# Optimization experiments

Measured on AMD Instinct MI355X. Metric: run time of the kernel, lower is better.

The kernel has to match this reference:

```python
import jax, jax.numpy as jnp
from jax import lax
import numpy as np

B, N, C, NPOINT, K = 8, 4096, 64, 1024, 32
EPS = 1e-5
SLOPE = 0.1  # leakyrelu negative_slope


def setup_inputs() -> dict:
    key = jax.random.key(0)
    ks = jax.random.split(key, 8)
    d = {
        "xyz": jax.random.normal(ks[0], (B, N, 3), jnp.float32),
        "features": jax.random.normal(ks[1], (B, N, C), jnp.float32),
    }
    for i, n in enumerate(["w_t", "w1_0", "w2_0", "w1_1", "w2_1"]):
        d[n] = jax.random.normal(ks[2 + i], (C, C), jnp.float32) * 0.05
    for n in ["b_t", "b1_0", "b2_0", "b1_1", "b2_1"]:
        d[n] = jnp.zeros((C,), jnp.float32)
    for n in ["g_t", "g1_0", "g2_0", "g1_1", "g2_1"]:
        d[n] = jnp.ones((C,), jnp.float32)
    for n in ["beta_t", "beta1_0", "beta2_0", "beta1_1", "beta2_1"]:
        d[n] = jnp.zeros((C,), jnp.float32)
    return d


def leaky(x):
    return jnp.where(x >= 0, x, SLOPE * x)


def conv1(x, w, b):  # x: [M, Cin, K], w: [Cout, Cin] (1x1 conv)
    return jnp.einsum('mck,oc->mok', x, w) + b[None, :, None]


def bn(x, g, be):  # training-mode BatchNorm1d over (batch, spatial)
    mean = x.mean(axis=(0, 2), keepdims=True)
    var = x.var(axis=(0, 2), keepdims=True)
    return g[None, :, None] * (x - mean) / jnp.sqrt(var + EPS) + be[None, :, None]


def fps(xyz, npoint):
    """Farthest point sampling, deterministic start at index 0. -> [B, npoint] int32"""
    b, n, _ = xyz.shape
    def step(carry, _):
        dist, far = carry
        centroid = jnp.take_along_axis(xyz, far[:, None, None], axis=1)  # [B,1,3]
        d = jnp.sum((xyz - centroid) ** 2, -1)  # [B,N]
        dist = jnp.minimum(dist, d)
        return (dist, jnp.argmax(dist, -1)), far
    init = (jnp.full((b, n), 1e10, xyz.dtype), jnp.zeros((b,), jnp.int32))
    _, idxs = lax.scan(step, init, None, length=npoint)  # [npoint, B]
    return idxs.T


def sqdist(src, dst):  # [B,S,3],[B,N,3] -> [B,S,N]
    d = -2.0 * jnp.einsum('bsc,bnc->bsn', src, dst)
    d += jnp.sum(src ** 2, -1)[:, :, None]
    d += jnp.sum(dst ** 2, -1)[:, None, :]
    return d


def resblock(x, w1, b1, g1, be1, w2, b2, g2, be2):
    h = leaky(bn(conv1(x, w1, b1), g1, be1))
    h = bn(conv1(h, w2, b2), g2, be2)
    return leaky(h + x)


def reference(xyz, features, w_t, b_t, g_t, beta_t,
              w1_0, b1_0, g1_0, beta1_0, w2_0, b2_0, g2_0, beta2_0,
              w1_1, b1_1, g1_1, beta1_1, w2_1, b2_1, g2_1, beta2_1):
    fps_idx = fps(xyz, NPOINT)                                   # [B,S]
    new_xyz = jnp.take_along_axis(xyz, fps_idx[:, :, None], axis=1)  # [B,S,3]
    d = sqdist(new_xyz, xyz)                                     # [B,S,N]
    _, idx = lax.top_k(-d, K)                                    # k smallest -> [B,S,K]
    grouped = jax.vmap(lambda f, i: f[i])(features, idx)         # [B,S,K,C]
    x = grouped.transpose(0, 1, 3, 2).reshape(B * NPOINT, C, K)  # [B*S, C, K]
    x = leaky(bn(conv1(x, w_t, b_t), g_t, beta_t))
    x = resblock(x, w1_0, b1_0, g1_0, beta1_0, w2_0, b2_0, g2_0, beta2_0)
    x = resblock(x, w1_1, b1_1, g1_1, beta1_1, w2_1, b2_1, g2_1, beta2_1)
    nf = x.reshape(B, NPOINT, C, K).transpose(0, 2, 1, 3)        # [B,C,S,K]
    sub_features = nf.max(axis=-1)                               # [B,C,S]
    return (new_xyz.transpose(0, 2, 1), sub_features)
```

## Files before the change

### kernel.cpp

```cpp
#include <hip/hip_runtime.h>
#include <stdint.h>

#define NB 8
#define NN 4096
#define NC 64
#define NS 1024
#define NK 32
#define NQ (NB*NS)
#define NP (NQ*NK)
#define EPSBN 1e-5f

typedef unsigned long long u64;
typedef unsigned short u16;
typedef float v2f __attribute__((ext_vector_type(2)));
typedef short bf8_t __attribute__((ext_vector_type(8)));
typedef float f4_t __attribute__((ext_vector_type(4)));

__device__ __forceinline__ float lrelu(float x){ return x >= 0.0f ? x : 0.1f*x; }

__device__ __forceinline__ unsigned int fkey(float d){
    unsigned int fb = __float_as_uint(d);
    return (fb & 0x80000000u) ? ~fb : (fb | 0x80000000u);
}
__device__ __forceinline__ unsigned f2bf(float f){
    unsigned u = __float_as_uint(f);
    return (u + 0x7fffu + ((u >> 16) & 1u)) >> 16;
}
__device__ __forceinline__ float bflo(unsigned u){ return __uint_as_float(u << 16); }
__device__ __forceinline__ float bfhi(unsigned u){ return __uint_as_float(u & 0xffff0000u); }

__device__ __forceinline__ int wave_incl_add(int x){
    int v = x;
    {int o=__builtin_amdgcn_update_dpp(0,v,0x111,0xf,0xf,true); v+=o;}
    {int o=__builtin_amdgcn_update_dpp(0,v,0x112,0xf,0xf,true); v+=o;}
    {int o=__builtin_amdgcn_update_dpp(0,v,0x114,0xf,0xf,true); v+=o;}
    {int o=__builtin_amdgcn_update_dpp(0,v,0x118,0xf,0xf,true); v+=o;}
    {int o=__builtin_amdgcn_update_dpp(0,v,0x142,0xa,0xf,true); v+=o;}
    {int o=__builtin_amdgcn_update_dpp(0,v,0x143,0xc,0xf,true); v+=o;}
    return v;
}
__device__ __forceinline__ float row_sum16(float x){
    int v = __float_as_int(x);
    {int o=__builtin_amdgcn_update_dpp(0,v,0x111,0xf,0xf,true); v=__float_as_int(__int_as_float(v)+__int_as_float(o));}
    {int o=__builtin_amdgcn_update_dpp(0,v,0x112,0xf,0xf,true); v=__float_as_int(__int_as_float(v)+__int_as_float(o));}
    {int o=__builtin_amdgcn_update_dpp(0,v,0x114,0xf,0xf,true); v=__float_as_int(__int_as_float(v)+__int_as_float(o));}
    {int o=__builtin_amdgcn_update_dpp(0,v,0x118,0xf,0xf,true); v=__float_as_int(__int_as_float(v)+__int_as_float(o));}
    return __int_as_float(v);
}
__device__ __forceinline__ double wave_max_d(double x){
    int lo = __double2loint(x), hi = __double2hiint(x);
    #define FPS_STG(ctl) { \
        int nl=__builtin_amdgcn_update_dpp(lo,lo,ctl,0xf,0xf,false); \
        int nh=__builtin_amdgcn_update_dpp(hi,hi,ctl,0xf,0xf,false); \
        double mx=fmax(__hiloint2double(hi,lo), __hiloint2double(nh,nl)); \
        lo=__double2loint(mx); hi=__double2hiint(mx); }
    FPS_STG(0x111) FPS_STG(0x112) FPS_STG(0x114) FPS_STG(0x118) FPS_STG(0x142) FPS_STG(0x143)
    #undef FPS_STG
    int flo = __builtin_amdgcn_readlane(lo, 63);
    int fhi = __builtin_amdgcn_readlane(hi, 63);
    return __hiloint2double(fhi, flo);
}

__global__ __launch_bounds__(256,1) void fps_kernel(const float* __restrict__ xyz,
                                                    float* __restrict__ out0,
                                                    float* __restrict__ nxyz)
{
    __shared__ float sX[NN], sY[NN], sZ[NN];
    __shared__ double slots[2][4];
    __shared__ int sFar[NS];
    const int b = blockIdx.x, t = threadIdx.x;
    const int lane = t & 63, wv = t >> 6;
    const float* base = xyz + (size_t)b*NN*3;
    for (int i = t; i < NN; i += 256){
        const float* pp = base + 3*i;
        sX[i] = pp[0]; sY[i] = pp[1]; sZ[i] = pp[2];
    }
    __syncthreads();
    v2f PX[8], PY[8], PZ[8], D[8];
    int LO[16];
    const int pb = t*16;
    #pragma unroll
    for (int j = 0; j < 8; ++j){
        PX[j] = (v2f){ sX[pb+2*j], sX[pb+2*j+1] };
        PY[j] = (v2f){ sY[pb+2*j], sY[pb+2*j+1] };
        PZ[j] = (v2f){ sZ[pb+2*j], sZ[pb+2*j+1] };
        D[j]  = (v2f){ 1e10f, 1e10f };
    }
    #pragma unroll
    for (int j = 0; j < 16; ++j) LO[j] = (int)(~(unsigned)(pb + j));
    int far = 0;
    float cx = sX[0], cy = sY[0], cz = sZ[0];
    for (int s = 0; s < NS; ++s){
        if (t == 255) sFar[s] = far;
        double best;
        {
            #pragma clang fp contract(off)
            v2f cx2 = (v2f){cx, cx}, cy2 = (v2f){cy, cy}, cz2 = (v2f){cz, cz};
            best = -1.0;
            #pragma unroll
            for (int j = 0; j < 8; ++j){
                v2f dx = PX[j] - cx2;
                v2f dy = PY[j] - cy2;
                v2f dz = PZ[j] - cz2;
                v2f dd = (dx*dx + dy*dy) + dz*dz;
                v2f nd = __builtin_elementwise_min(D[j], dd);
                D[j] = nd;
                best = fmax(best, __hiloint2double(__float_as_int(nd.x), LO[2*j]));
                best = fmax(best, __hiloint2double(__float_as_int(nd.y), LO[2*j+1]));
            }
        }
        double wb = wave_max_d(best);
        const int par = s & 1;
        if (lane == 0) slots[par][wv] = wb;
        __syncthreads();
        double s0 = slots[par][0], s1 = slots[par][1];
        double s2 = slots[par][2], s3 = slots[par][3];
        double mm = fmax(fmax(s0, s1), fmax(s2, s3));
        far = (int)(~(unsigned)__double2loint(mm));
        cx = sX[far]; cy = sY[far]; cz = sZ[far];
    }
    __syncthreads();
    for (int s = t; s < NS; s += 256){
        const int f = sFar[s];
        const float x = sX[f], y = sY[f], z = sZ[f];
        float* npq = nxyz + ((size_t)b*NS + s)*3;
        npq[0]=x; npq[1]=y; npq[2]=z;
        out0[(b*3+0)*NS+s]=x; out0[(b*3+1)*NS+s]=y; out0[(b*3+2)*NS+s]=z;
    }
}

__global__ __launch_bounds__(256,2) void knn_kernel(const float* __restrict__ xyz,
                                                    const float* __restrict__ nxyz,
                                                    int* __restrict__ kidx)
{
    const int t = threadIdx.x, lane = t & 63, w = t >> 6;
    const int q = blockIdx.x*4 + w;
    const int b = q >> 10;
    const float* base = xyz + (size_t)b*NN*3;
    const float* qp = nxyz + (size_t)q*3;
    const float qx = qp[0], qy = qp[1], qz = qp[2];
    const float qsq = __fadd_rn(__fadd_rn(__fmul_rn(qx,qx),__fmul_rn(qy,qy)),__fmul_rn(qz,qz));

    unsigned int key[64];
    #pragma unroll
    for (int i = 0; i < 64; ++i){
        const int idx = (i<<6) + lane;
        const float* pp = base + 3*idx;
        float x = pp[0], y = pp[1], z = pp[2];
        float dot = __fadd_rn(__fadd_rn(__fmul_rn(qx,x),__fmul_rn(qy,y)),__fmul_rn(qz,z));
        float psq = __fadd_rn(__fadd_rn(__fmul_rn(x,x),__fmul_rn(y,y)),__fmul_rn(z,z));
        float d = __fadd_rn(__fadd_rn(__fmul_rn(-2.0f,dot),qsq),psq);
        key[i] = fkey(d);
    }
    unsigned int pref = 0; int need = 32;
    for (int bit = 31; bit >= 0; --bit){
        const unsigned int bound = 1u << bit;
        int c = 0;
        #pragma unroll
        for (int i = 0; i < 64; ++i) c += ((key[i] ^ pref) < bound) ? 1 : 0;
        int tot = __builtin_amdgcn_readlane(wave_incl_add(c), 63);
        if (tot < need){ need -= tot; pref |= bound; }
    }
    const unsigned int T = pref;
    int cl = 0;
    #pragma unroll
    for (int i = 0; i < 64; ++i) cl += (key[i] < T) ? 1 : 0;
    int incl_cl = wave_incl_add(cl);
    int clx = incl_cl - cl;
    int tiebase = __builtin_amdgcn_readlane(incl_cl, 63);
    int* oq = kidx + (size_t)q*NK;
    int pos = clx;
    #pragma unroll
    for (int i = 0; i < 64; ++i){
        if (key[i] < T){ oq[pos] = (i<<6) + lane; ++pos; }
    }
    int tcount = 0;
    for (int i = 0; i < 64 && tcount < need; ++i){
        u64 m = __ballot(key[i] == T);
        int myrank = (int)__popcll(m & ((1ull << lane) - 1ull));
        if ((key[i] == T) && (tcount + myrank < need))
            oq[tiebase + tcount + myrank] = (i<<6) + lane;
        tcount += (int)__popcll(m);
    }
}

__global__ __launch_bounds__(256) void wtrans_kernel(const float* __restrict__ w0,
    const float* __restrict__ w1, const float* __restrict__ w2,
    const float* __restrict__ w3, const float* __restrict__ w4,
    u16* __restrict__ dst)
{
    const float* s;
    switch (blockIdx.x){
        case 0: s = w0; break; case 1: s = w1; break; case 2: s = w2; break;
        case 3: s = w3; break; default: s = w4; break;
    }
    u16* d = dst + (size_t)blockIdx.x*4096;
    for (int i = threadIdx.x; i < 4096; i += 256){
        const int f = i >> 9, lane = (i >> 3) & 63, j = i & 7;
        const int mt = f >> 1, h = f & 1;
        const int o = mt*16 + (lane & 15);
        const int c = h*32 + (lane >> 4)*8 + j;
        d[i] = (u16)f2bf(s[o*64 + c]);
    }
}

__global__ __launch_bounds__(1024) void finalize_kernel(const float* __restrict__ pin,
    const float* __restrict__ g, const float* __restrict__ beta, float* __restrict__ aff)
{
    __shared__ float l1[1024];
    const int t = threadIdx.x;
    const int stat = t & 127, seg = t >> 7;
    float S = 0.0f;
    #pragma unroll 8
    for (int r = seg*128; r < seg*128 + 128; ++r) S += pin[r*128 + stat];
    l1[t] = S;
    __syncthreads();
    if (t < 128){
        float s = l1[t] + l1[128+t] + l1[256+t] + l1[384+t]
                + l1[512+t] + l1[640+t] + l1[768+t] + l1[896+t];
        l1[t] = s;
    }
    __syncthreads();
    if (t < 64){
        float mean = l1[t] * (1.0f/(float)NP);
        float var  = fmaxf(l1[64+t] * (1.0f/(float)NP) - mean*mean, 0.0f);
        float sc = g[t] * rsqrtf(var + EPSBN);
        aff[t]    = sc;
        aff[64+t] = beta[t] - mean*sc;
    }
}

template<int ACT>
__global__ __launch_bounds__(256,3) void conv_mfma_kernel(const u16* __restrict__ in,
    u16* __restrict__ out, const u16* __restrict__ wfrag, const float* __restrict__ bias,
    const float* __restrict__ aff, float* __restrict__ pout)
{
    __shared__ float sStat[4*128];
    const int t = threadIdx.x, lane = t & 63, wv = t >> 6;
    const int n = lane & 15, q = lane >> 4;
    const int bb = blockIdx.x;

    float scr[16], shr[16];
    if (ACT){
        #pragma unroll
        for (int h = 0; h < 2; ++h){
            float4 a0 = *(const float4*)(aff + h*32 + q*8);
            float4 a1 = *(const float4*)(aff + h*32 + q*8 + 4);
            float4 b0 = *(const float4*)(aff + 64 + h*32 + q*8);
            float4 b1 = *(const float4*)(aff + 64 + h*32 + q*8 + 4);
            scr[h*8+0]=a0.x; scr[h*8+1]=a0.y; scr[h*8+2]=a0.z; scr[h*8+3]=a0.w;
            scr[h*8+4]=a1.x; scr[h*8+5]=a1.y; scr[h*8+6]=a1.z; scr[h*8+7]=a1.w;
            shr[h*8+0]=b0.x; shr[h*8+1]=b0.y; shr[h*8+2]=b0.z; shr[h*8+3]=b0.w;
            shr[h*8+4]=b1.x; shr[h*8+5]=b1.y; shr[h*8+6]=b1.z; shr[h*8+7]=b1.w;
        }
    }
    bf8_t wf[8];
    #pragma unroll
    for (int f = 0; f < 8; ++f)
        wf[f] = *(const bf8_t*)(wfrag + (f*64 + lane)*8);
    f4_t bv[4];
    #pragma unroll
    for (int mt = 0; mt < 4; ++mt)
        bv[mt] = *(const f4_t*)(bias + mt*16 + q*4);

    float st1[16], st2[16];
    #pragma unroll
    for (int e = 0; e < 16; ++e){ st1[e] = 0.0f; st2[e] = 0.0f; }

    #pragma unroll
    for (int i = 0; i < 4; ++i){
        const int p0 = bb*256 + wv*64 + i*16;
        const u16* row = in + (size_t)(p0 + n)*64;
        bf8_t bf0, bf1;
        if (ACT){
            union { unsigned u[4]; bf8_t v; } B0, B1;
            uint4 r0 = *(const uint4*)(row + q*8);
            uint4 r1 = *(const uint4*)(row + 32 + q*8);
            const unsigned ra[4] = {r0.x, r0.y, r0.z, r0.w};
            const unsigned rb[4] = {r1.x, r1.y, r1.z, r1.w};
            #pragma unroll
            for (int d = 0; d < 4; ++d){
                float x0 = bflo(ra[d]), x1 = bfhi(ra[d]);
                float y0 = fmaf(scr[2*d],   x0, shr[2*d]);   y0 = lrelu(y0);
                float y1 = fmaf(scr[2*d+1], x1, shr[2*d+1]); y1 = lrelu(y1);
                B0.u[d] = f2bf(y0) | (f2bf(y1) << 16);
                float z0 = bflo(rb[d]), z1 = bfhi(rb[d]);
                float w0 = fmaf(scr[8+2*d],   z0, shr[8+2*d]);   w0 = lrelu(w0);
                float w1 = fmaf(scr[8+2*d+1], z1, shr[8+2*d+1]); w1 = lrelu(w1);
                B1.u[d] = f2bf(w0) | (f2bf(w1) << 16);
            }
            bf0 = B0.v; bf1 = B1.v;
        } else {
            bf0 = *(const bf8_t*)(row + q*8);
            bf1 = *(const bf8_t*)(row + 32 + q*8);
        }
        f4_t acc[4];
        #pragma unroll
        for (int mt = 0; mt < 4; ++mt){
            acc[mt] = (f4_t){0.f,0.f,0.f,0.f};
            acc[mt] = __builtin_amdgcn_mfma_f32_16x16x32_bf16(wf[mt*2+0], bf0, acc[mt], 0,0,0);
            acc[mt] = __builtin_amdgcn_mfma_f32_16x16x32_bf16(wf[mt*2+1], bf1, acc[mt], 0,0,0);
        }
        u16* orow = out + (size_t)(p0 + n)*64;
        #pragma unroll
        for (int mt = 0; mt < 4; ++mt){
            float v0 = acc[mt].x + bv[mt].x;
            float v1 = acc[mt].y + bv[mt].y;
            float v2 = acc[mt].z + bv[mt].z;
            float v3 = acc[mt].w + bv[mt].w;
            st1[mt*4+0] += v0; st2[mt*4+0] += v0*v0;
            st1[mt*4+1] += v1; st2[mt*4+1] += v1*v1;
            st1[mt*4+2] += v2; st2[mt*4+2] += v2*v2;
            st1[mt*4+3] += v3; st2[mt*4+3] += v3*v3;
            uint2 pk;
            pk.x = f2bf(v0) | (f2bf(v1) << 16);
            pk.y = f2bf(v2) | (f2bf(v3) << 16);
            *(uint2*)(orow + mt*16 + q*4) = pk;
        }
    }
    #pragma unroll
    for (int e = 0; e < 16; ++e){
        float r1 = row_sum16(st1[e]);
        float r2 = row_sum16(st2[e]);
        if (n == 15){
            const int ch = (e >> 2)*16 + q*4 + (e & 3);
            sStat[wv*128 + ch]      = r1;
            sStat[wv*128 + 64 + ch] = r2;
        }
    }
    __syncthreads();
    if (t < 128){
        float s = sStat[t] + sStat[128+t] + sStat[256+t] + sStat[384+t];
        pout[(size_t)bb*128 + t] = s;
    }
}

__global__ __launch_bounds__(256,3) void gconv_mfma_kernel(const float* __restrict__ features,
    const int* __restrict__ kidx, u16* __restrict__ out,
    const u16* __restrict__ wfrag, const float* __restrict__ bias,
    float* __restrict__ pout)
{
    __shared__ float sStat[4*128];
    const int t = threadIdx.x, lane = t & 63, wv = t >> 6;
    const int n = lane & 15, q = lane >> 4;
    const int bb = blockIdx.x;

    bf8_t wf[8];
    #pragma unroll
    for (int f = 0; f < 8; ++f)
        wf[f] = *(const bf8_t*)(wfrag + (f*64 + lane)*8);
    f4_t bv[4];
    #pragma unroll
    for (int mt = 0; mt < 4; ++mt)
        bv[mt] = *(const f4_t*)(bias + mt*16 + q*4);

    float st1[16], st2[16];
    #pragma unroll
    for (int e = 0; e < 16; ++e){ st1[e] = 0.0f; st2[e] = 0.0f; }

    #pragma unroll
    for (int i = 0; i < 4; ++i){
        const int p0 = bb*256 + wv*64 + i*16;
        const int p = p0 + n;
        const int b = p >> 15;
        const int idx = kidx[p];
        const float* frow = features + ((size_t)b*NN + idx)*NC;
        union { unsigned u[4]; bf8_t v; } B0, B1;
        {
            float4 a0 = *(const float4*)(frow + q*8);
            float4 a1 = *(const float4*)(frow + q*8 + 4);
            B0.u[0] = f2bf(a0.x) | (f2bf(a0.y) << 16);
            B0.u[1] = f2bf(a0.z) | (f2bf(a0.w) << 16);
            B0.u[2] = f2bf(a1.x) | (f2bf(a1.y) << 16);
            B0.u[3] = f2bf(a1.z) | (f2bf(a1.w) << 16);
            float4 c0 = *(const float4*)(frow + 32 + q*8);
            float4 c1 = *(const float4*)(frow + 32 + q*8 + 4);
            B1.u[0] = f2bf(c0.x) | (f2bf(c0.y) << 16);
            B1.u[1] = f2bf(c0.z) | (f2bf(c0.w) << 16);
            B1.u[2] = f2bf(c1.x) | (f2bf(c1.y) << 16);
            B1.u[3] = f2bf(c1.z) | (f2bf(c1.w) << 16);
        }
        f4_t acc[4];
        #pragma unroll
        for (int mt = 0; mt < 4; ++mt){
            acc[mt] = (f4_t){0.f,0.f,0.f,0.f};
            acc[mt] = __builtin_amdgcn_mfma_f32_16x16x32_bf16(wf[mt*2+0], B0.v, acc[mt], 0,0,0);
            acc[mt] = __builtin_amdgcn_mfma_f32_16x16x32_bf16(wf[mt*2+1], B1.v, acc[mt], 0,0,0);
        }
        u16* orow = out + (size_t)p*64;
        #pragma unroll
        for (int mt = 0; mt < 4; ++mt){
            float v0 = acc[mt].x + bv[mt].x;
            float v1 = acc[mt].y + bv[mt].y;
            float v2 = acc[mt].z + bv[mt].z;
            float v3 = acc[mt].w + bv[mt].w;
            st1[mt*4+0] += v0; st2[mt*4+0] += v0*v0;
            st1[mt*4+1] += v1; st2[mt*4+1] += v1*v1;
            st1[mt*4+2] += v2; st2[mt*4+2] += v2*v2;
            st1[mt*4+3] += v3; st2[mt*4+3] += v3*v3;
            uint2 pk;
            pk.x = f2bf(v0) | (f2bf(v1) << 16);
            pk.y = f2bf(v2) | (f2bf(v3) << 16);
            *(uint2*)(orow + mt*16 + q*4) = pk;
        }
    }
    #pragma unroll
    for (int e = 0; e < 16; ++e){
        float r1 = row_sum16(st1[e]);
        float r2 = row_sum16(st2[e]);
        if (n == 15){
            const int ch = (e >> 2)*16 + q*4 + (e & 3);
            sStat[wv*128 + ch]      = r1;
            sStat[wv*128 + 64 + ch] = r2;
        }
    }
    __syncthreads();
    if (t < 128){
        float s = sStat[t] + sStat[128+t] + sStat[256+t] + sStat[384+t];
        pout[(size_t)bb*128 + t] = s;
    }
}

__global__ __launch_bounds__(256,2) void resid_kernel(const u16* __restrict__ v,
    const u16* __restrict__ yt, u16* __restrict__ x2,
    const float* __restrict__ affV, const float* __restrict__ affY)
{
    const int t = threadIdx.x;
    const int dc = t & 31, rg = t >> 5;
    const int c0 = dc*2, c1 = c0 + 1;
    const float va0 = affV[c0], vb0 = affV[64+c0];
    const float va1 = affV[c1], vb1 = affV[64+c1];
    const float ya0 = affY[c0], yb0 = affY[64+c0];
    const float ya1 = affY[c1], yb1 = affY[64+c1];
    const unsigned* vp = (const unsigned*)v;
    const unsigned* yp = (const unsigned*)yt;
    unsigned* xp = (unsigned*)x2;
    const size_t base = (size_t)blockIdx.x*512;
    #pragma unroll 4
    for (int r = rg; r < 512; r += 8){
        const size_t e = (base + r)*32 + dc;
        unsigned uv = vp[e], uy = yp[e];
        float r0 = lrelu(fmaf(va0, bflo(uv), vb0) + lrelu(fmaf(ya0, bflo(uy), yb0)));
        float r1 = lrelu(fmaf(va1, bfhi(uv), vb1) + lrelu(fmaf(ya1, bfhi(uy), yb1)));
        xp[e] = f2bf(r0) | (f2bf(r1) << 16);
    }
}

__global__ __launch_bounds__(256,2) void final_kernel(const u16* __restrict__ v2,
    const u16* __restrict__ x2, const float* __restrict__ aff,
    float* __restrict__ out1)
{
    const int t = threadIdx.x;
    const int dc = t & 31, sg = t >> 5;
    const int c0 = dc*2, c1 = c0 + 1;
    const float a0 = aff[c0], s0 = aff[64+c0];
    const float a1 = aff[c1], s1 = aff[64+c1];
    const int s = blockIdx.x*8 + sg;
    const unsigned* vp = (const unsigned*)v2;
    const unsigned* xp = (const unsigned*)x2;
    float m0 = -3.0e38f, m1 = -3.0e38f;
    #pragma unroll 8
    for (int kk = 0; kk < 32; ++kk){
        const size_t e = ((size_t)s*32 + kk)*32 + dc;
        unsigned uv = vp[e], ux = xp[e];
        m0 = fmaxf(m0, lrelu(fmaf(a0, bflo(uv), s0) + bflo(ux)));
        m1 = fmaxf(m1, lrelu(fmaf(a1, bfhi(uv), s1) + bfhi(ux)));
    }
    const int b = s >> 10, sl = s & 1023;
    out1[((size_t)b*NC + c0)*NS + sl] = m0;
    out1[((size_t)b*NC + c1)*NS + sl] = m1;
}

extern "C" void kernel_launch(void* const* d_in, const int* in_sizes, int n_in,
                              void* d_out, int out_size, void* d_ws, size_t ws_size,
                              hipStream_t stream)
{
    const float* xyz      = (const float*)d_in[0];
    const float* features = (const float*)d_in[1];
    const float* w_t    = (const float*)d_in[2];
    const float* w1_0   = (const float*)d_in[3];
    const float* w2_0   = (const float*)d_in[4];
    const float* w1_1   = (const float*)d_in[5];
    const float* w2_1   = (const float*)d_in[6];
    const float* b_t    = (const float*)d_in[7];
    const float* b1_0   = (const float*)d_in[8];
    const float* b2_0   = (const float*)d_in[9];
    const float* b1_1   = (const float*)d_in[10];
    const float* b2_1   = (const float*)d_in[11];
    const float* g_t    = (const float*)d_in[12];
    const float* g1_0   = (const float*)d_in[13];
    const float* g2_0   = (const float*)d_in[14];
    const float* g1_1   = (const float*)d_in[15];
    const float* g2_1   = (const float*)d_in[16];
    const float* beta_t  = (const float*)d_in[17];
    const float* beta1_0 = (const float*)d_in[18];
    const float* beta2_0 = (const float*)d_in[19];
    const float* beta1_1 = (const float*)d_in[20];
    const float* beta2_1 = (const float*)d_in[21];

    float* out = (float*)d_out;

    float* nxyz = (float*)d_ws;
    int*   kidx = (int*)(nxyz + 24576);
    float* pT   = (float*)(kidx + NP);
    float* p10  = pT  + 131072;
    float* p20  = p10 + 131072;
    float* p11  = p20 + 131072;
    float* p21  = p11 + 131072;
    float* affT  = p21 + 131072;
    float* aff10 = affT + 128;
    float* aff20 = aff10 + 128;
    float* aff11 = aff20 + 128;
    float* aff21 = aff11 + 128;
    u16*  bwt  = (u16*)(aff21 + 128);
    u16*  buf0 = bwt + 5*4096;
    u16*  buf1 = buf0 + (size_t)NP*NC;
    u16*  buf2 = buf1 + (size_t)NP*NC;

    wtrans_kernel<<<5, 256, 0, stream>>>(w_t, w1_0, w2_0, w1_1, w2_1, bwt);
    fps_kernel<<<NB, 256, 0, stream>>>(xyz, out, nxyz);
    knn_kernel<<<NQ/4, 256, 0, stream>>>(xyz, nxyz, kidx);

    gconv_mfma_kernel<<<1024, 256, 0, stream>>>(features, kidx, buf1,
                                                bwt + 0*4096, b_t, pT);
    finalize_kernel<<<1, 1024, 0, stream>>>(pT, g_t, beta_t, affT);
    conv_mfma_kernel<1><<<1024, 256, 0, stream>>>(buf1, buf0, bwt + 1*4096, b1_0,
                                                  affT, p10);
    finalize_kernel<<<1, 1024, 0, stream>>>(p10, g1_0, beta1_0, aff10);
    conv_mfma_kernel<1><<<1024, 256, 0, stream>>>(buf0, buf2, bwt + 2*4096, b2_0,
                                                  aff10, p20);
    finalize_kernel<<<1, 1024, 0, stream>>>(p20, g2_0, beta2_0, aff20);
    resid_kernel<<<512, 256, 0, stream>>>(buf2, buf1, buf0, aff20, affT);
    conv_mfma_kernel<0><<<1024, 256, 0, stream>>>(buf0, buf1, bwt + 3*4096, b1_1,
                                                  nullptr, p11);
    finalize_kernel<<<1, 1024, 0, stream>>>(p11, g1_1, beta1_1, aff11);
    conv_mfma_kernel<1><<<1024, 256, 0, stream>>>(buf1, buf2, bwt + 4*4096, b2_1,
                                                  aff11, p21);
    finalize_kernel<<<1, 1024, 0, stream>>>(p21, g2_1, beta2_1, aff21);
    final_kernel<<<1024, 256, 0, stream>>>(buf2, buf0, aff21,
                                           out + (size_t)NB*3*NS);
}
```

Baseline: 931.5 us.

## Replace BN finalize kernels with atomic stat sums and in-kernel affine prologue

Each conv kernel now accumulates its batch-norm statistics with atomicAdd into a single 128-float buffer, zeroed by the weight-transform kernel, instead of writing per-block partials. The separate finalize launches are removed, and each consumer kernel computes the scale and shift in a shared-memory prologue. This removes five single-block launches and their serialization points, at the cost of 1024 blocks contending on 128 atomics and float summation order that varies from run to run. FPS also switches to a float4 shared-memory layout and splits its max reduction across four accumulators to shorten the dependency chain.

```diff
diff --git a/kernel.cpp b/kernel.cpp
--- a/kernel.cpp
+++ b/kernel.cpp
@@ -65,7 +65,7 @@
                                                     float* __restrict__ out0,
                                                     float* __restrict__ nxyz)
 {
-    __shared__ float sX[NN], sY[NN], sZ[NN];
+    __shared__ float4 sP[NN];
     __shared__ double slots[2][4];
     __shared__ int sFar[NS];
     const int b = blockIdx.x, t = threadIdx.x;
@@ -73,7 +73,7 @@
     const float* base = xyz + (size_t)b*NN*3;
     for (int i = t; i < NN; i += 256){
         const float* pp = base + 3*i;
-        sX[i] = pp[0]; sY[i] = pp[1]; sZ[i] = pp[2];
+        sP[i] = (float4){pp[0], pp[1], pp[2], 0.0f};
     }
     __syncthreads();
     v2f PX[8], PY[8], PZ[8], D[8];
@@ -81,22 +81,23 @@
     const int pb = t*16;
     #pragma unroll
     for (int j = 0; j < 8; ++j){
-        PX[j] = (v2f){ sX[pb+2*j], sX[pb+2*j+1] };
-        PY[j] = (v2f){ sY[pb+2*j], sY[pb+2*j+1] };
-        PZ[j] = (v2f){ sZ[pb+2*j], sZ[pb+2*j+1] };
+        float4 p0 = sP[pb+2*j], p1 = sP[pb+2*j+1];
+        PX[j] = (v2f){ p0.x, p1.x };
+        PY[j] = (v2f){ p0.y, p1.y };
+        PZ[j] = (v2f){ p0.z, p1.z };
         D[j]  = (v2f){ 1e10f, 1e10f };
     }
     #pragma unroll
     for (int j = 0; j < 16; ++j) LO[j] = (int)(~(unsigned)(pb + j));
     int far = 0;
-    float cx = sX[0], cy = sY[0], cz = sZ[0];
+    float cx = sP[0].x, cy = sP[0].y, cz = sP[0].z;
     for (int s = 0; s < NS; ++s){
         if (t == 255) sFar[s] = far;
         double best;
         {
             #pragma clang fp contract(off)
             v2f cx2 = (v2f){cx, cx}, cy2 = (v2f){cy, cy}, cz2 = (v2f){cz, cz};
-            best = -1.0;
+            double b0 = -1.0, b1 = -1.0, b2 = -1.0, b3 = -1.0;
             #pragma unroll
             for (int j = 0; j < 8; ++j){
                 v2f dx = PX[j] - cx2;
@@ -105,9 +106,12 @@
                 v2f dd = (dx*dx + dy*dy) + dz*dz;
                 v2f nd = __builtin_elementwise_min(D[j], dd);
                 D[j] = nd;
-                best = fmax(best, __hiloint2double(__float_as_int(nd.x), LO[2*j]));
-                best = fmax(best, __hiloint2double(__float_as_int(nd.y), LO[2*j+1]));
+                double k0 = __hiloint2double(__float_as_int(nd.x), LO[2*j]);
+                double k1 = __hiloint2double(__float_as_int(nd.y), LO[2*j+1]);
+                if (j & 1){ b1 = fmax(b1, k0); b3 = fmax(b3, k1); }
+                else      { b0 = fmax(b0, k0); b2 = fmax(b2, k1); }
             }
+            best = fmax(fmax(b0, b1), fmax(b2, b3));
         }
         double wb = wave_max_d(best);
         const int par = s & 1;
@@ -117,15 +121,16 @@
         double s2 = slots[par][2], s3 = slots[par][3];
         double mm = fmax(fmax(s0, s1), fmax(s2, s3));
         far = (int)(~(unsigned)__double2loint(mm));
-        cx = sX[far]; cy = sY[far]; cz = sZ[far];
+        float4 cc = sP[far];
+        cx = cc.x; cy = cc.y; cz = cc.z;
     }
     __syncthreads();
     for (int s = t; s < NS; s += 256){
         const int f = sFar[s];
-        const float x = sX[f], y = sY[f], z = sZ[f];
+        float4 cc = sP[f];
         float* npq = nxyz + ((size_t)b*NS + s)*3;
-        npq[0]=x; npq[1]=y; npq[2]=z;
-        out0[(b*3+0)*NS+s]=x; out0[(b*3+1)*NS+s]=y; out0[(b*3+2)*NS+s]=z;
+        npq[0]=cc.x; npq[1]=cc.y; npq[2]=cc.z;
+        out0[(b*3+0)*NS+s]=cc.x; out0[(b*3+1)*NS+s]=cc.y; out0[(b*3+2)*NS+s]=cc.z;
     }
 }
 
@@ -187,13 +192,15 @@
 __global__ __launch_bounds__(256) void wtrans_kernel(const float* __restrict__ w0,
     const float* __restrict__ w1, const float* __restrict__ w2,
     const float* __restrict__ w3, const float* __restrict__ w4,
-    u16* __restrict__ dst)
+    u16* __restrict__ dst, float* __restrict__ sums)
 {
     const float* s;
     switch (blockIdx.x){
         case 0: s = w0; break; case 1: s = w1; break; case 2: s = w2; break;
         case 3: s = w3; break; default: s = w4; break;
     }
+    for (int i = threadIdx.x; i < 128; i += 256)
+        sums[(size_t)blockIdx.x*128 + i] = 0.0f;
     u16* d = dst + (size_t)blockIdx.x*4096;
     for (int i = threadIdx.x; i < 4096; i += 256){
         const int f = i >> 9, lane = (i >> 3) & 63, j = i & 7;
@@ -204,50 +211,41 @@
     }
 }
 
-__global__ __launch_bounds__(1024) void finalize_kernel(const float* __restrict__ pin,
-    const float* __restrict__ g, const float* __restrict__ beta, float* __restrict__ aff)
-{
-    __shared__ float l1[1024];
-    const int t = threadIdx.x;
-    const int stat = t & 127, seg = t >> 7;
-    float S = 0.0f;
-    #pragma unroll 8
-    for (int r = seg*128; r < seg*128 + 128; ++r) S += pin[r*128 + stat];
-    l1[t] = S;
-    __syncthreads();
-    if (t < 128){
-        float s = l1[t] + l1[128+t] + l1[256+t] + l1[384+t]
-                + l1[512+t] + l1[640+t] + l1[768+t] + l1[896+t];
-        l1[t] = s;
-    }
-    __syncthreads();
+__device__ __forceinline__ void bn_affine_prologue(const float* __restrict__ sums,
+    const float* __restrict__ g, const float* __restrict__ beta, float* sAff, int t)
+{
     if (t < 64){
-        float mean = l1[t] * (1.0f/(float)NP);
-        float var  = fmaxf(l1[64+t] * (1.0f/(float)NP) - mean*mean, 0.0f);
+        float su = sums[t], sq = sums[64+t];
+        float mean = su * (1.0f/(float)NP);
+        float var  = fmaxf(sq * (1.0f/(float)NP) - mean*mean, 0.0f);
         float sc = g[t] * rsqrtf(var + EPSBN);
-        aff[t]    = sc;
-        aff[64+t] = beta[t] - mean*sc;
+        sAff[t]    = sc;
+        sAff[64+t] = beta[t] - mean*sc;
     }
 }
 
 template<int ACT>
 __global__ __launch_bounds__(256,3) void conv_mfma_kernel(const u16* __restrict__ in,
     u16* __restrict__ out, const u16* __restrict__ wfrag, const float* __restrict__ bias,
-    const float* __restrict__ aff, float* __restrict__ pout)
+    const float* __restrict__ sums, const float* __restrict__ g,
+    const float* __restrict__ beta, float* __restrict__ pout)
 {
     __shared__ float sStat[4*128];
+    __shared__ float sAff[128];
     const int t = threadIdx.x, lane = t & 63, wv = t >> 6;
     const int n = lane & 15, q = lane >> 4;
     const int bb = blockIdx.x;
 
     float scr[16], shr[16];
     if (ACT){
+        bn_affine_prologue(sums, g, beta, sAff, t);
+        __syncthreads();
         #pragma unroll
         for (int h = 0; h < 2; ++h){
-            float4 a0 = *(const float4*)(aff + h*32 + q*8);
-            float4 a1 = *(const float4*)(aff + h*32 + q*8 + 4);
-            float4 b0 = *(const float4*)(aff + 64 + h*32 + q*8);
-            float4 b1 = *(const float4*)(aff + 64 + h*32 + q*8 + 4);
+            float4 a0 = *(const float4*)(sAff + h*32 + q*8);
+            float4 a1 = *(const float4*)(sAff + h*32 + q*8 + 4);
+            float4 b0 = *(const float4*)(sAff + 64 + h*32 + q*8);
+            float4 b1 = *(const float4*)(sAff + 64 + h*32 + q*8 + 4);
             scr[h*8+0]=a0.x; scr[h*8+1]=a0.y; scr[h*8+2]=a0.z; scr[h*8+3]=a0.w;
             scr[h*8+4]=a1.x; scr[h*8+5]=a1.y; scr[h*8+6]=a1.z; scr[h*8+7]=a1.w;
             shr[h*8+0]=b0.x; shr[h*8+1]=b0.y; shr[h*8+2]=b0.z; shr[h*8+3]=b0.w;
@@ -331,7 +329,7 @@
     __syncthreads();
     if (t < 128){
         float s = sStat[t] + sStat[128+t] + sStat[256+t] + sStat[384+t];
-        pout[(size_t)bb*128 + t] = s;
+        atomicAdd(pout + t, s);
     }
 }
 
@@ -417,21 +415,26 @@
     __syncthreads();
     if (t < 128){
         float s = sStat[t] + sStat[128+t] + sStat[256+t] + sStat[384+t];
-        pout[(size_t)bb*128 + t] = s;
+        atomicAdd(pout + t, s);
     }
 }
 
 __global__ __launch_bounds__(256,2) void resid_kernel(const u16* __restrict__ v,
     const u16* __restrict__ yt, u16* __restrict__ x2,
-    const float* __restrict__ affV, const float* __restrict__ affY)
-{
+    const float* __restrict__ sumsV, const float* __restrict__ gV, const float* __restrict__ betaV,
+    const float* __restrict__ sumsY, const float* __restrict__ gY, const float* __restrict__ betaY)
+{
+    __shared__ float sAV[128], sAY[128];
     const int t = threadIdx.x;
+    bn_affine_prologue(sumsV, gV, betaV, sAV, t);
+    if (t >= 64 && t < 128) bn_affine_prologue(sumsY, gY, betaY, sAY, t - 64);
+    __syncthreads();
     const int dc = t & 31, rg = t >> 5;
     const int c0 = dc*2, c1 = c0 + 1;
-    const float va0 = affV[c0], vb0 = affV[64+c0];
-    const float va1 = affV[c1], vb1 = affV[64+c1];
-    const float ya0 = affY[c0], yb0 = affY[64+c0];
-    const float ya1 = affY[c1], yb1 = affY[64+c1];
+    const float va0 = sAV[c0], vb0 = sAV[64+c0];
+    const float va1 = sAV[c1], vb1 = sAV[64+c1];
+    const float ya0 = sAY[c0], yb0 = sAY[64+c0];
+    const float ya1 = sAY[c1], yb1 = sAY[64+c1];
     const unsigned* vp = (const unsigned*)v;
     const unsigned* yp = (const unsigned*)yt;
     unsigned* xp = (unsigned*)x2;
@@ -447,14 +450,18 @@
 }
 
 __global__ __launch_bounds__(256,2) void final_kernel(const u16* __restrict__ v2,
-    const u16* __restrict__ x2, const float* __restrict__ aff,
+    const u16* __restrict__ x2,
+    const float* __restrict__ sums, const float* __restrict__ g, const float* __restrict__ beta,
     float* __restrict__ out1)
 {
+    __shared__ float sAff[128];
     const int t = threadIdx.x;
+    bn_affine_prologue(sums, g, beta, sAff, t);
+    __syncthreads();
     const int dc = t & 31, sg = t >> 5;
     const int c0 = dc*2, c1 = c0 + 1;
-    const float a0 = aff[c0], s0 = aff[64+c0];
-    const float a1 = aff[c1], s1 = aff[64+c1];
+    const float a0 = sAff[c0], s0 = sAff[64+c0];
+    const float a1 = sAff[c1], s1 = sAff[64+c1];
     const int s = blockIdx.x*8 + sg;
     const unsigned* vp = (const unsigned*)v2;
     const unsigned* xp = (const unsigned*)x2;
@@ -502,41 +509,36 @@
 
     float* nxyz = (float*)d_ws;
     int*   kidx = (int*)(nxyz + 24576);
-    float* pT   = (float*)(kidx + NP);
-    float* p10  = pT  + 131072;
-    float* p20  = p10 + 131072;
-    float* p11  = p20 + 131072;
-    float* p21  = p11 + 131072;
-    float* affT  = p21 + 131072;
-    float* aff10 = affT + 128;
-    float* aff20 = aff10 + 128;
-    float* aff11 = aff20 + 128;
-    float* aff21 = aff11 + 128;
-    u16*  bwt  = (u16*)(aff21 + 128);
+    float* sums = (float*)(kidx + NP);
+    u16*  bwt  = (u16*)(sums + 5*128);
     u16*  buf0 = bwt + 5*4096;
     u16*  buf1 = buf0 + (size_t)NP*NC;
     u16*  buf2 = buf1 + (size_t)NP*NC;
 
-    wtrans_kernel<<<5, 256, 0, stream>>>(w_t, w1_0, w2_0, w1_1, w2_1, bwt);
+    float* sumsT  = sums + 0*128;
+    float* sums10 = sums + 1*128;
+    float* sums20 = sums + 2*128;
+    float* sums11 = sums + 3*128;
+    float* sums21 = sums + 4*128;
+
+    wtrans_kernel<<<5, 256, 0, stream>>>(w_t, w1_0, w2_0, w1_1, w2_1, bwt, sums);
     fps_kernel<<<NB, 256, 0, stream>>>(xyz, out, nxyz);
     knn_kernel<<<NQ/4, 256, 0, stream>>>(xyz, nxyz, kidx);
 
     gconv_mfma_kernel<<<1024, 256, 0, stream>>>(features, kidx, buf1,
-                                                bwt + 0*4096, b_t, pT);
-    finalize_kernel<<<1, 1024, 0, stream>>>(pT, g_t, beta_t, affT);
+                                                bwt + 0*4096, b_t, sumsT);
     conv_mfma_kernel<1><<<1024, 256, 0, stream>>>(buf1, buf0, bwt + 1*4096, b1_0,
-                                                  affT, p10);
-    finalize_kernel<<<1, 1024, 0, stream>>>(p10, g1_0, beta1_0, aff10);
+                                                  sumsT, g_t, beta_t, sums10);
     conv_mfma_kernel<1><<<1024, 256, 0, stream>>>(buf0, buf2, bwt + 2*4096, b2_0,
-                                                  aff10, p20);
-    finalize_kernel<<<1, 1024, 0, stream>>>(p20, g2_0, beta2_0, aff20);
-    resid_kernel<<<512, 256, 0, stream>>>(buf2, buf1, buf0, aff20, affT);
+                                                  sums10, g1_0, beta1_0, sums20);
+    resid_kernel<<<512, 256, 0, stream>>>(buf2, buf1, buf0,
+                                          sums20, g2_0, beta2_0,
+                                          sumsT, g_t, beta_t);
     conv_mfma_kernel<0><<<1024, 256, 0, stream>>>(buf0, buf1, bwt + 3*4096, b1_1,
-                                                  nullptr, p11);
-    finalize_kernel<<<1, 1024, 0, stream>>>(p11, g1_1, beta1_1, aff11);
+                                                  nullptr, nullptr, nullptr, sums11);
     conv_mfma_kernel<1><<<1024, 256, 0, stream>>>(buf1, buf2, bwt + 4*4096, b2_1,
-                                                  aff11, p21);
-    finalize_kernel<<<1, 1024, 0, stream>>>(p21, g2_1, beta2_1, aff21);
-    final_kernel<<<1024, 256, 0, stream>>>(buf2, buf0, aff21,
+                                                  sums11, g1_1, beta1_1, sums21);
+    final_kernel<<<1024, 256, 0, stream>>>(buf2, buf0,
+                                           sums21, g2_1, beta2_1,
                                            out + (size_t)NB*3*NS);
 }
```

Measured after the change: 1.010 ms. 1.08x slower.
